# Kernel optimization log

Hardware: AMD Instinct MI355X
Metric: run time of the kernel (lower is better)

Reference implementation:

```python
import jax, jax.numpy as jnp
import numpy as np

SEQ = 4096
EMB = 2048
DQ = 2048
DV = 2048

def setup_inputs() -> dict:
    key = jax.random.key(0)
    k1, k2, k3, k4 = jax.random.split(key, 4)
    scale = 1.0 / np.sqrt(EMB)
    return {
        "embedding_word": jax.random.normal(k1, (SEQ, EMB), dtype=jnp.float32),
        "w_q": jax.random.normal(k2, (DQ, EMB), dtype=jnp.float32) * scale,
        "w_k": jax.random.normal(k3, (DQ, EMB), dtype=jnp.float32) * scale,
        "w_v": jax.random.normal(k4, (DV, EMB), dtype=jnp.float32) * scale,
    }

def reference(embedding_word, w_q, w_k, w_v):
    # nn.Linear: y = x @ W.T (bias=False)
    q = embedding_word @ w_q.T            # [S, d_q]
    k = embedding_word @ w_k.T            # [S, d_q]
    v = embedding_word @ w_v.T            # [S, d_v]
    scores = q @ k.T                      # [S, S]
    S = scores.shape[0]
    causal = jnp.tril(jnp.ones((S, S), dtype=bool))  # True = keep
    masked = jnp.where(causal, scores, -jnp.inf)
    weights = jax.nn.softmax(masked / jnp.sqrt(jnp.float32(DQ)), axis=-1)
    return weights @ v                    # [S, d_v]
```

## Files before the change

### kernel.cpp

```cpp
#include <hip/hip_runtime.h>


using u16 = unsigned short;
typedef __bf16 bf16x8 __attribute__((ext_vector_type(8)));
typedef float  f32x4  __attribute__((ext_vector_type(4)));
typedef u16    u16x8  __attribute__((ext_vector_type(8)));

__device__ __forceinline__ u16 f2b(float f) {
  union { float f; unsigned u; } x; x.f = f;
  unsigned r = x.u + 0x7fffu + ((x.u >> 16) & 1u);
  return (u16)(r >> 16);
}
__device__ __forceinline__ float b2f(u16 h) {
  union { unsigned u; float f; } x; x.u = ((unsigned)h) << 16;
  return x.f;
}

#define GLL16(src, dst)                                                        \
  __builtin_amdgcn_global_load_lds(                                            \
      (const __attribute__((address_space(1))) void*)(src),                    \
      (__attribute__((address_space(3))) void*)(dst), 16, 0, 0)

#define MFMA_BF16(a, b, c) __builtin_amdgcn_mfma_f32_16x16x32_bf16(a, b, c, 0, 0, 0)

__global__ __launch_bounds__(256)
void cast_all(const float* __restrict__ x, const float* __restrict__ wq,
              const float* __restrict__ wk, const float* __restrict__ wv,
              u16* __restrict__ dst) {
  const int b = blockIdx.x;
  const float* src;
  size_t off;
  if (b < 4096)      { src = x;  off = (size_t)b * 2048; }
  else if (b < 6144) { src = wq; off = (size_t)(b - 4096) * 2048; }
  else if (b < 8192) { src = wk; off = (size_t)(b - 6144) * 2048; }
  else               { src = wv; off = (size_t)(b - 8192) * 2048; }
  const size_t e = off + (size_t)threadIdx.x * 8;
  float4 a = *(const float4*)(src + e);
  float4 c = *(const float4*)(src + e + 4);
  u16x8 o;
  o[0] = f2b(a.x); o[1] = f2b(a.y); o[2] = f2b(a.z); o[3] = f2b(a.w);
  o[4] = f2b(c.x); o[5] = f2b(c.y); o[6] = f2b(c.z); o[7] = f2b(c.w);
  *(u16x8*)(dst + (size_t)b * 2048 + (size_t)threadIdx.x * 8) = o;
}

__global__ __launch_bounds__(512)
void gemm_qkv(const u16* __restrict__ A, const u16* __restrict__ W,
              u16* __restrict__ Qo, u16* __restrict__ Ko,
              u16* __restrict__ VTo, int bn_base) {
  extern __shared__ char lds[];
  constexpr int NT = 32;
  const int bn = blockIdx.x + bn_base, bm = blockIdx.y;
  const int tid = threadIdx.x;
  const int w = tid >> 6, lane = tid & 63;
  const int wr = w >> 1, wc = w & 1;
  const int l15 = lane & 15, l4 = lane >> 4;
  const int rs = lane >> 3;
  const int csw = ((lane & 7) ^ rs) << 3;
  const int m0 = bm * 256, n0 = bn * 128;

  const u16* gA = A + (size_t)(m0 + w * 8 + rs) * 2048 + csw;
  const u16* gB = W + (size_t)(n0 + w * 8 + rs) * 2048 + csw;
  char* lw = lds + w * 1024;
  const u16* sm = (const u16*)lds;

  auto stA = [&](int p, int u, int tt) {
    GLL16(gA + (size_t)u * 64 * 2048 + tt * 64, lw + p * 49152 + u * 8192);
  };
  auto stB = [&](int p, int u, int tt) {
    GLL16(gB + (size_t)u * 64 * 2048 + tt * 64, lw + p * 49152 + 32768 + u * 8192);
  };
  const int swz = (l15 & 7) << 3;
  auto rdA = [&](int p, int m, int kk) -> bf16x8 {
    int e = p * 24576 + wr * 4096 + (((m * 16 + l15) * 64 + kk * 32 + l4 * 8) ^ swz);
    return *(const bf16x8*)&sm[e];
  };
  auto rdB = [&](int p, int n, int kk) -> bf16x8 {
    int e = p * 24576 + 16384 + wc * 4096 +
            (((n * 16 + l15) * 64 + kk * 32 + l4 * 8) ^ swz);
    return *(const bf16x8*)&sm[e];
  };

  f32x4 acc[4][4] = {};
  bf16x8 aE[4][2], aO[4][2], b01E[2][2], b01O[2][2], b23E[2][2], b23O[2][2];

  stA(0,0,0); stA(0,1,0); stA(0,2,0); stA(0,3,0); stB(0,0,0); stB(0,1,0);
  stA(1,0,1); stA(1,1,1); stA(1,2,1); stA(1,3,1); stB(1,0,1); stB(1,1,1);
  asm volatile("s_waitcnt vmcnt(6)" ::: "memory");
  __builtin_amdgcn_sched_barrier(0);
  __builtin_amdgcn_s_barrier();
#pragma unroll
  for (int m = 0; m < 4; ++m) { aE[m][0] = rdA(0,m,0); aE[m][1] = rdA(0,m,1); }
#pragma unroll
  for (int n = 0; n < 2; ++n) { b01E[n][0] = rdB(0,n,0); b01E[n][1] = rdB(0,n,1); }
  asm volatile("s_waitcnt lgkmcnt(0)" ::: "memory");
  __builtin_amdgcn_sched_barrier(0);
  __builtin_amdgcn_s_barrier();

  for (int i = 0; i < NT / 2; ++i) {
    const int te = 2 * i, to = 2 * i + 1;
    if (te + 2 < NT) { stA(0,0,te+2); stA(0,1,te+2); stA(0,2,te+2); }
#pragma unroll
    for (int n = 0; n < 2; ++n) { b23E[n][0] = rdB(0,n+2,0); b23E[n][1] = rdB(0,n+2,1); }
    __builtin_amdgcn_s_barrier();
    __builtin_amdgcn_s_setprio(1);
#pragma unroll
    for (int m = 0; m < 4; ++m)
#pragma unroll
      for (int n = 0; n < 2; ++n)
#pragma unroll
        for (int kk = 0; kk < 2; ++kk)
          acc[m][n] = MFMA_BF16(aE[m][kk], b01E[n][kk], acc[m][n]);
    __builtin_amdgcn_s_setprio(0);
    asm volatile("s_waitcnt lgkmcnt(0)" ::: "memory");
    __builtin_amdgcn_sched_barrier(0);
    __builtin_amdgcn_s_barrier();
    if (te + 2 < NT) {
      stA(0,3,te+2); stB(0,0,te+2); stB(0,1,te+2);
      asm volatile("s_waitcnt vmcnt(6)" ::: "memory");
    } else {
      asm volatile("s_waitcnt vmcnt(0)" ::: "memory");
    }
    __builtin_amdgcn_sched_barrier(0);
    __builtin_amdgcn_s_barrier();
#pragma unroll
    for (int m = 0; m < 4; ++m) { aO[m][0] = rdA(1,m,0); aO[m][1] = rdA(1,m,1); }
#pragma unroll
    for (int n = 0; n < 2; ++n) { b01O[n][0] = rdB(1,n,0); b01O[n][1] = rdB(1,n,1); }
    __builtin_amdgcn_s_setprio(1);
#pragma unroll
    for (int m = 0; m < 4; ++m)
#pragma unroll
      for (int n = 0; n < 2; ++n)
#pragma unroll
        for (int kk = 0; kk < 2; ++kk)
          acc[m][n+2] = MFMA_BF16(aE[m][kk], b23E[n][kk], acc[m][n+2]);
    __builtin_amdgcn_s_setprio(0);
    asm volatile("s_waitcnt lgkmcnt(0)" ::: "memory");
    __builtin_amdgcn_sched_barrier(0);
    __builtin_amdgcn_s_barrier();
    if (to + 2 < NT) { stA(1,0,to+2); stA(1,1,to+2); stA(1,2,to+2); }
#pragma unroll
    for (int n = 0; n < 2; ++n) { b23O[n][0] = rdB(1,n+2,0); b23O[n][1] = rdB(1,n+2,1); }
    __builtin_amdgcn_s_barrier();
    __builtin_amdgcn_s_setprio(1);
#pragma unroll
    for (int m = 0; m < 4; ++m)
#pragma unroll
      for (int n = 0; n < 2; ++n)
#pragma unroll
        for (int kk = 0; kk < 2; ++kk)
          acc[m][n] = MFMA_BF16(aO[m][kk], b01O[n][kk], acc[m][n]);
    __builtin_amdgcn_s_setprio(0);
    asm volatile("s_waitcnt lgkmcnt(0)" ::: "memory");
    __builtin_amdgcn_sched_barrier(0);
    __builtin_amdgcn_s_barrier();
    if (to + 2 < NT) {
      stA(1,3,to+2); stB(1,0,to+2); stB(1,1,to+2);
      asm volatile("s_waitcnt vmcnt(6)" ::: "memory");
    } else if (to + 1 < NT) {
      asm volatile("s_waitcnt vmcnt(0)" ::: "memory");
    }
    __builtin_amdgcn_sched_barrier(0);
    __builtin_amdgcn_s_barrier();
    if (to + 1 < NT) {
#pragma unroll
      for (int m = 0; m < 4; ++m) { aE[m][0] = rdA(0,m,0); aE[m][1] = rdA(0,m,1); }
#pragma unroll
      for (int n = 0; n < 2; ++n) { b01E[n][0] = rdB(0,n,0); b01E[n][1] = rdB(0,n,1); }
    }
    __builtin_amdgcn_s_setprio(1);
#pragma unroll
    for (int m = 0; m < 4; ++m)
#pragma unroll
      for (int n = 0; n < 2; ++n)
#pragma unroll
        for (int kk = 0; kk < 2; ++kk)
          acc[m][n+2] = MFMA_BF16(aO[m][kk], b23O[n][kk], acc[m][n+2]);
    __builtin_amdgcn_s_setprio(0);
    asm volatile("s_waitcnt lgkmcnt(0)" ::: "memory");
    __builtin_amdgcn_sched_barrier(0);
    __builtin_amdgcn_s_barrier();
  }

  const int row0 = m0 + wr * 64 + l4 * 4;
  const int cg0 = n0 + wc * 64 + l15;
  if (bn < 16) {
#pragma unroll
    for (int m = 0; m < 4; ++m)
#pragma unroll
      for (int n = 0; n < 4; ++n)
#pragma unroll
        for (int j = 0; j < 4; ++j)
          Qo[(size_t)(row0 + m * 16 + j) * 2048 + cg0 + n * 16] = f2b(acc[m][n][j]);
  } else if (bn < 32) {
#pragma unroll
    for (int m = 0; m < 4; ++m)
#pragma unroll
      for (int n = 0; n < 4; ++n)
#pragma unroll
        for (int j = 0; j < 4; ++j)
          Ko[(size_t)(row0 + m * 16 + j) * 2048 + (cg0 + n * 16 - 2048)] = f2b(acc[m][n][j]);
  } else {
#pragma unroll
    for (int m = 0; m < 4; ++m)
#pragma unroll
      for (int n = 0; n < 4; ++n)
#pragma unroll
        for (int j = 0; j < 4; ++j)
          VTo[(size_t)(cg0 + n * 16 - 4096) * 4096 + row0 + m * 16 + j] = f2b(acc[m][n][j]);
  }
}

template<int MODE>
__global__ __launch_bounds__(256)
void pipe128(const u16* __restrict__ A, const u16* __restrict__ B,
             void* __restrict__ C, float alpha) {
  extern __shared__ char lds[];
  constexpr int LDA = (MODE == 0) ? 2048 : 4096;
  constexpr int LDB = (MODE == 0) ? 2048 : 4096;

  int bm, bn;
  if (MODE == 0) {
    const int b = blockIdx.x;
    int r = (int)((sqrtf(8.f * (float)b + 1.f) - 1.f) * 0.5f);
    while ((r + 1) * (r + 2) / 2 <= b) ++r;
    while (r * (r + 1) / 2 > b) --r;
    bm = r; bn = b - r * (r + 1) / 2;
  } else {
    const int b = blockIdx.x;
    bm = (b < 256) ? (b >> 4) : (31 - ((b - 256) >> 4));
    bn = b & 15;
  }
  const int NT = (MODE == 0) ? 32 : 2 * (bm + 1);

  const int tid = threadIdx.x;
  const int w = tid >> 6, lane = tid & 63;
  const int wr = w >> 1, wc = w & 1;
  const int l15 = lane & 15, l4 = lane >> 4;
  const int rs = lane >> 3;
  const int csw = ((lane & 7) ^ rs) << 3;
  const int m0 = bm * 128, n0 = bn * 128;

  const u16* gA = A + (size_t)(m0 + w * 8 + rs) * LDA + csw;
  const u16* gB = B + (size_t)(n0 + w * 8 + rs) * LDB + csw;
  char* lw = lds + w * 1024;
  const u16* sm = (const u16*)lds;

  auto stA = [&](int p, int u, int tt) {
    GLL16(gA + (size_t)(u * 32) * LDA + tt * 64, lw + p * 32768 + u * 4096);
  };
  auto stB = [&](int p, int u, int tt) {
    GLL16(gB + (size_t)(u * 32) * LDB + tt * 64, lw + p * 32768 + 16384 + u * 4096);
  };
  const int swz = (l15 & 7) << 3;
  auto rdA = [&](int p, int m, int kk) -> bf16x8 {
    int e = p * 16384 + wr * 4096 + (((m * 16 + l15) * 64 + kk * 32 + l4 * 8) ^ swz);
    return *(const bf16x8*)&sm[e];
  };
  auto rdB = [&](int p, int n, int kk) -> bf16x8 {
    int e = p * 16384 + 8192 + wc * 4096 +
            (((n * 16 + l15) * 64 + kk * 32 + l4 * 8) ^ swz);
    return *(const bf16x8*)&sm[e];
  };

  f32x4 acc[4][4] = {};
  bf16x8 aE[4][2], aO[4][2], b01E[2][2], b01O[2][2], b23E[2][2], b23O[2][2];

  stA(0,0,0); stA(0,1,0); stA(0,2,0); stA(0,3,0);
  stB(0,0,0); stB(0,1,0); stB(0,2,0); stB(0,3,0);
  stA(1,0,1); stA(1,1,1); stA(1,2,1); stA(1,3,1);
  stB(1,0,1); stB(1,1,1); stB(1,2,1); stB(1,3,1);
  asm volatile("s_waitcnt vmcnt(8)" ::: "memory");
  __builtin_amdgcn_sched_barrier(0);
  __builtin_amdgcn_s_barrier();
#pragma unroll
  for (int m = 0; m < 4; ++m) { aE[m][0] = rdA(0,m,0); aE[m][1] = rdA(0,m,1); }
#pragma unroll
  for (int n = 0; n < 2; ++n) { b01E[n][0] = rdB(0,n,0); b01E[n][1] = rdB(0,n,1); }
  asm volatile("s_waitcnt lgkmcnt(0)" ::: "memory");
  __builtin_amdgcn_sched_barrier(0);
  __builtin_amdgcn_s_barrier();

  for (int i = 0; i < (NT >> 1); ++i) {
    const int te = 2 * i, to = 2 * i + 1;
    if (te + 2 < NT) { stA(0,0,te+2); stA(0,1,te+2); stA(0,2,te+2); stA(0,3,te+2); }
#pragma unroll
    for (int n = 0; n < 2; ++n) { b23E[n][0] = rdB(0,n+2,0); b23E[n][1] = rdB(0,n+2,1); }
    __builtin_amdgcn_s_barrier();
    __builtin_amdgcn_s_setprio(1);
#pragma unroll
    for (int m = 0; m < 4; ++m)
#pragma unroll
      for (int n = 0; n < 2; ++n)
#pragma unroll
        for (int kk = 0; kk < 2; ++kk)
          acc[m][n] = MFMA_BF16(aE[m][kk], b01E[n][kk], acc[m][n]);
    __builtin_amdgcn_s_setprio(0);
    asm volatile("s_waitcnt lgkmcnt(0)" ::: "memory");
    __builtin_amdgcn_sched_barrier(0);
    __builtin_amdgcn_s_barrier();
    if (te + 2 < NT) {
      stB(0,0,te+2); stB(0,1,te+2); stB(0,2,te+2); stB(0,3,te+2);
      asm volatile("s_waitcnt vmcnt(8)" ::: "memory");
    } else {
      asm volatile("s_waitcnt vmcnt(0)" ::: "memory");
    }
    __builtin_amdgcn_sched_barrier(0);
    __builtin_amdgcn_s_barrier();
#pragma unroll
    for (int m = 0; m < 4; ++m) { aO[m][0] = rdA(1,m,0); aO[m][1] = rdA(1,m,1); }
#pragma unroll
    for (int n = 0; n < 2; ++n) { b01O[n][0] = rdB(1,n,0); b01O[n][1] = rdB(1,n,1); }
    __builtin_amdgcn_s_setprio(1);
#pragma unroll
    for (int m = 0; m < 4; ++m)
#pragma unroll
      for (int n = 0; n < 2; ++n)
#pragma unroll
        for (int kk = 0; kk < 2; ++kk)
          acc[m][n+2] = MFMA_BF16(aE[m][kk], b23E[n][kk], acc[m][n+2]);
    __builtin_amdgcn_s_setprio(0);
    asm volatile("s_waitcnt lgkmcnt(0)" ::: "memory");
    __builtin_amdgcn_sched_barrier(0);
    __builtin_amdgcn_s_barrier();
    if (to + 2 < NT) { stA(1,0,to+2); stA(1,1,to+2); stA(1,2,to+2); stA(1,3,to+2); }
#pragma unroll
    for (int n = 0; n < 2; ++n) { b23O[n][0] = rdB(1,n+2,0); b23O[n][1] = rdB(1,n+2,1); }
    __builtin_amdgcn_s_barrier();
    __builtin_amdgcn_s_setprio(1);
#pragma unroll
    for (int m = 0; m < 4; ++m)
#pragma unroll
      for (int n = 0; n < 2; ++n)
#pragma unroll
        for (int kk = 0; kk < 2; ++kk)
          acc[m][n] = MFMA_BF16(aO[m][kk], b01O[n][kk], acc[m][n]);
    __builtin_amdgcn_s_setprio(0);
    asm volatile("s_waitcnt lgkmcnt(0)" ::: "memory");
    __builtin_amdgcn_sched_barrier(0);
    __builtin_amdgcn_s_barrier();
    if (to + 2 < NT) {
      stB(1,0,to+2); stB(1,1,to+2); stB(1,2,to+2); stB(1,3,to+2);
      asm volatile("s_waitcnt vmcnt(8)" ::: "memory");
    } else if (to + 1 < NT) {
      asm volatile("s_waitcnt vmcnt(0)" ::: "memory");
    }
    __builtin_amdgcn_sched_barrier(0);
    __builtin_amdgcn_s_barrier();
    if (to + 1 < NT) {
#pragma unroll
      for (int m = 0; m < 4; ++m) { aE[m][0] = rdA(0,m,0); aE[m][1] = rdA(0,m,1); }
#pragma unroll
      for (int n = 0; n < 2; ++n) { b01E[n][0] = rdB(0,n,0); b01E[n][1] = rdB(0,n,1); }
    }
    __builtin_amdgcn_s_setprio(1);
#pragma unroll
    for (int m = 0; m < 4; ++m)
#pragma unroll
      for (int n = 0; n < 2; ++n)
#pragma unroll
        for (int kk = 0; kk < 2; ++kk)
          acc[m][n+2] = MFMA_BF16(aO[m][kk], b23O[n][kk], acc[m][n+2]);
    __builtin_amdgcn_s_setprio(0);
    asm volatile("s_waitcnt lgkmcnt(0)" ::: "memory");
    __builtin_amdgcn_sched_barrier(0);
    __builtin_amdgcn_s_barrier();
  }

  const int row0 = m0 + wr * 64 + l4 * 4;
  const int col0 = n0 + wc * 64 + l15;
  if (MODE == 0) {
    u16* Co = (u16*)C;
#pragma unroll
    for (int m = 0; m < 4; ++m)
#pragma unroll
      for (int n = 0; n < 4; ++n)
#pragma unroll
        for (int j = 0; j < 4; ++j)
          Co[(size_t)(row0 + m * 16 + j) * 4096 + col0 + n * 16] =
              f2b(acc[m][n][j] * alpha);
  } else {
    float* Co = (float*)C;
#pragma unroll
    for (int m = 0; m < 4; ++m)
#pragma unroll
      for (int n = 0; n < 4; ++n)
#pragma unroll
        for (int j = 0; j < 4; ++j)
          Co[(size_t)(row0 + m * 16 + j) * 2048 + col0 + n * 16] = acc[m][n][j];
  }
}

__global__ __launch_bounds__(256)
void softmax_causal(u16* __restrict__ S) {
  const int i = blockIdx.x;
  const int t = threadIdx.x;
  u16* row = S + (size_t)i * 4096;

  u16x8 r0 = *(const u16x8*)(row + t * 16);
  u16x8 r1 = *(const u16x8*)(row + t * 16 + 8);

  float v[16];
  float mx = -__builtin_inff();
#pragma unroll
  for (int c = 0; c < 16; ++c) {
    int j = t * 16 + c;
    float x = b2f(c < 8 ? r0[c] : r1[c - 8]);
    v[c] = (j <= i) ? x : -__builtin_inff();
    mx = fmaxf(mx, v[c]);
  }
#pragma unroll
  for (int off = 32; off >= 1; off >>= 1) mx = fmaxf(mx, __shfl_xor(mx, off));
  __shared__ float red[8];
  if ((t & 63) == 0) red[t >> 6] = mx;
  __syncthreads();
  mx = fmaxf(fmaxf(red[0], red[1]), fmaxf(red[2], red[3]));

  float s = 0.f;
#pragma unroll
  for (int c = 0; c < 16; ++c) {
    float e = exp2f((v[c] - mx) * 1.4426950408889634f);
    v[c] = e;
    s += e;
  }
#pragma unroll
  for (int off = 32; off >= 1; off >>= 1) s += __shfl_xor(s, off);
  if ((t & 63) == 0) red[4 + (t >> 6)] = s;
  __syncthreads();
  s = red[4] + red[5] + red[6] + red[7];
  float inv = 1.0f / s;

  u16x8 o0, o1;
#pragma unroll
  for (int c = 0; c < 8; ++c) {
    o0[c] = f2b(v[c] * inv);
    o1[c] = f2b(v[c + 8] * inv);
  }
  *(u16x8*)(row + t * 16) = o0;
  *(u16x8*)(row + t * 16 + 8) = o1;
}

extern "C" void kernel_launch(void* const* d_in, const int* in_sizes, int n_in,
                              void* d_out, int out_size, void* d_ws, size_t ws_size,
                              hipStream_t stream) {
  const float* x  = (const float*)d_in[0];
  const float* wq = (const float*)d_in[1];
  const float* wk = (const float*)d_in[2];
  const float* wv = (const float*)d_in[3];

  u16* x_bf  = (u16*)d_ws;
  u16* wq_bf = x_bf  + (size_t)4096 * 2048;
  u16* K_bf  = wq_bf + (size_t)3 * 2048 * 2048;
  u16* VT_bf = K_bf  + (size_t)4096 * 2048;
  u16* S_bf  = VT_bf + (size_t)2048 * 4096;
  u16* Q_bf  = (u16*)d_out;

  const float alpha = 0.022097086912079612f;

  cast_all<<<dim3(10240), 256, 0, stream>>>(x, wq, wk, wv, x_bf);

  gemm_qkv<<<dim3(32, 16), 512, 98304, stream>>>(x_bf, wq_bf, Q_bf, K_bf, VT_bf, 0);
  pipe128<0><<<dim3(528), 256, 65536, stream>>>(Q_bf, K_bf, S_bf, alpha);
  gemm_qkv<<<dim3(16, 16), 512, 98304, stream>>>(x_bf, wq_bf, Q_bf, K_bf, VT_bf, 32);
  softmax_causal<<<dim3(4096), 256, 0, stream>>>(S_bf);
  pipe128<1><<<dim3(512), 256, 65536, stream>>>(S_bf, VT_bf, d_out, 1.0f);
}
```

Measured before the change: 252.4 us.

## Use 256x256 tiles for Q/K projection and interleave PV block order

Adds a new Q/K projection GEMM kernel that computes 256x256 output tiles with 8 waves in a 2x4 layout, replacing the 256x128 tile launch. The larger tile raises arithmetic intensity and cuts the number of blocks from 512 to 256, at the cost of 128KB LDS per block and a larger accumulator register footprint. Separately, the weights@V kernel now alternates short and long causal row blocks in launch order to balance the load across CUs.

```diff
diff --git a/kernel.cpp b/kernel.cpp
--- a/kernel.cpp
+++ b/kernel.cpp
@@ -44,6 +44,146 @@
 }
 
 __global__ __launch_bounds__(512)
+void gemm_qk256(const u16* __restrict__ A, const u16* __restrict__ W,
+                u16* __restrict__ Qo, u16* __restrict__ Ko) {
+  extern __shared__ char lds[];
+  constexpr int NT = 32;
+  const int bn = blockIdx.x, bm = blockIdx.y;
+  const int tid = threadIdx.x;
+  const int w = tid >> 6, lane = tid & 63;
+  const int wr = w >> 2, wc = w & 3;
+  const int l15 = lane & 15, l4 = lane >> 4;
+  const int rs = lane >> 3;
+  const int csw = ((lane & 7) ^ rs) << 3;
+  const int m0 = bm * 256, n0 = bn * 256;
+
+  const u16* gA = A + (size_t)(m0 + w * 8 + rs) * 2048 + csw;
+  const u16* gB = W + (size_t)(n0 + w * 8 + rs) * 2048 + csw;
+  char* lw = lds + w * 1024;
+  const u16* sm = (const u16*)lds;
+
+  auto stA = [&](int p, int u, int tt) {
+    GLL16(gA + (size_t)(u * 64) * 2048 + tt * 64, lw + p * 65536 + u * 8192);
+  };
+  auto stB = [&](int p, int u, int tt) {
+    GLL16(gB + (size_t)(u * 64) * 2048 + tt * 64,
+          lw + p * 65536 + 32768 + u * 8192);
+  };
+  const int swz = (l15 & 7) << 3;
+  auto rdA = [&](int p, int m, int kk) -> bf16x8 {
+    int u = wr * 2 + (m >> 2);
+    int r64 = (m & 3) * 16 + l15;
+    int e = p * 32768 + u * 4096 + ((r64 * 64 + kk * 32 + l4 * 8) ^ swz);
+    return *(const bf16x8*)&sm[e];
+  };
+  auto rdB = [&](int p, int n, int kk) -> bf16x8 {
+    int e = p * 32768 + 16384 + wc * 4096 +
+            (((n * 16 + l15) * 64 + kk * 32 + l4 * 8) ^ swz);
+    return *(const bf16x8*)&sm[e];
+  };
+
+  f32x4 acc[8][4] = {};
+  bf16x8 a0[4][2], a1[4][2], b0[2][2], b1[2][2];
+
+  stA(0,0,0); stA(0,1,0); stA(0,2,0); stA(0,3,0);
+  stB(0,0,0); stB(0,1,0); stB(0,2,0); stB(0,3,0);
+  stA(1,0,1); stA(1,1,1); stA(1,2,1); stA(1,3,1);
+  stB(1,0,1); stB(1,1,1); stB(1,2,1); stB(1,3,1);
+  asm volatile("s_waitcnt vmcnt(8)" ::: "memory");
+  __builtin_amdgcn_sched_barrier(0);
+  __builtin_amdgcn_s_barrier();
+
+  for (int t = 0; t < NT; ++t) {
+    const int p = t & 1;
+    const bool pre = (t + 2 < NT);
+#pragma unroll
+    for (int m = 0; m < 4; ++m) { a0[m][0] = rdA(p, m, 0); a0[m][1] = rdA(p, m, 1); }
+#pragma unroll
+    for (int n = 0; n < 2; ++n) { b0[n][0] = rdB(p, n, 0); b0[n][1] = rdB(p, n, 1); }
+    __builtin_amdgcn_s_barrier();
+    asm volatile("s_waitcnt lgkmcnt(0)" ::: "memory");
+    __builtin_amdgcn_sched_barrier(0);
+    __builtin_amdgcn_s_setprio(1);
+#pragma unroll
+    for (int m = 0; m < 4; ++m)
+#pragma unroll
+      for (int n = 0; n < 2; ++n)
+#pragma unroll
+        for (int kk = 0; kk < 2; ++kk)
+          acc[m][n] = MFMA_BF16(a0[m][kk], b0[n][kk], acc[m][n]);
+    __builtin_amdgcn_s_setprio(0);
+    __builtin_amdgcn_s_barrier();
+    if (pre) { stA(p, 0, t + 2); stA(p, 2, t + 2); }
+#pragma unroll
+    for (int n = 0; n < 2; ++n) { b1[n][0] = rdB(p, n + 2, 0); b1[n][1] = rdB(p, n + 2, 1); }
+    __builtin_amdgcn_s_barrier();
+    asm volatile("s_waitcnt lgkmcnt(0)" ::: "memory");
+    __builtin_amdgcn_sched_barrier(0);
+    __builtin_amdgcn_s_setprio(1);
+#pragma unroll
+    for (int m = 0; m < 4; ++m)
+#pragma unroll
+      for (int n = 0; n < 2; ++n)
+#pragma unroll
+        for (int kk = 0; kk < 2; ++kk)
+          acc[m][n + 2] = MFMA_BF16(a0[m][kk], b1[n][kk], acc[m][n + 2]);
+    __builtin_amdgcn_s_setprio(0);
+    __builtin_amdgcn_s_barrier();
+    if (pre) { stB(p, 0, t + 2); stB(p, 1, t + 2); }
+#pragma unroll
+    for (int m = 0; m < 4; ++m) { a1[m][0] = rdA(p, m + 4, 0); a1[m][1] = rdA(p, m + 4, 1); }
+    __builtin_amdgcn_s_barrier();
+    asm volatile("s_waitcnt lgkmcnt(0)" ::: "memory");
+    __builtin_amdgcn_sched_barrier(0);
+    __builtin_amdgcn_s_setprio(1);
+#pragma unroll
+    for (int m = 0; m < 4; ++m)
+#pragma unroll
+      for (int n = 0; n < 2; ++n)
+#pragma unroll
+        for (int kk = 0; kk < 2; ++kk)
+          acc[m + 4][n] = MFMA_BF16(a1[m][kk], b0[n][kk], acc[m + 4][n]);
+    __builtin_amdgcn_s_setprio(0);
+    __builtin_amdgcn_s_barrier();
+    if (pre) { stA(p, 1, t + 2); stA(p, 3, t + 2); stB(p, 2, t + 2); stB(p, 3, t + 2); }
+    __builtin_amdgcn_s_setprio(1);
+#pragma unroll
+    for (int m = 0; m < 4; ++m)
+#pragma unroll
+      for (int n = 0; n < 2; ++n)
+#pragma unroll
+        for (int kk = 0; kk < 2; ++kk)
+          acc[m + 4][n + 2] = MFMA_BF16(a1[m][kk], b1[n][kk], acc[m + 4][n + 2]);
+    __builtin_amdgcn_s_setprio(0);
+    if (pre)                { asm volatile("s_waitcnt vmcnt(8)" ::: "memory"); }
+    else if (t + 1 < NT)    { asm volatile("s_waitcnt vmcnt(0)" ::: "memory"); }
+    __builtin_amdgcn_sched_barrier(0);
+    __builtin_amdgcn_s_barrier();
+  }
+
+  const int row0 = m0 + wr * 128 + l4 * 4;
+  if (bn < 8) {
+    const int cg0 = bn * 256 + wc * 64 + l15;
+#pragma unroll
+    for (int m = 0; m < 8; ++m)
+#pragma unroll
+      for (int n = 0; n < 4; ++n)
+#pragma unroll
+        for (int j = 0; j < 4; ++j)
+          Qo[(size_t)(row0 + m * 16 + j) * 2048 + cg0 + n * 16] = f2b(acc[m][n][j]);
+  } else {
+    const int cg0 = bn * 256 - 2048 + wc * 64 + l15;
+#pragma unroll
+    for (int m = 0; m < 8; ++m)
+#pragma unroll
+      for (int n = 0; n < 4; ++n)
+#pragma unroll
+        for (int j = 0; j < 4; ++j)
+          Ko[(size_t)(row0 + m * 16 + j) * 2048 + cg0 + n * 16] = f2b(acc[m][n][j]);
+  }
+}
+
+__global__ __launch_bounds__(512)
 void gemm_qkv(const u16* __restrict__ A, const u16* __restrict__ W,
               u16* __restrict__ Qo, u16* __restrict__ Ko,
               u16* __restrict__ VTo, int bn_base) {
@@ -228,8 +368,9 @@
     bm = r; bn = b - r * (r + 1) / 2;
   } else {
     const int b = blockIdx.x;
-    bm = (b < 256) ? (b >> 4) : (31 - ((b - 256) >> 4));
-    bn = b & 15;
+    const int i = b >> 1;
+    bm = (b & 1) ? (31 - (i >> 4)) : (i >> 4);
+    bn = i & 15;
   }
   const int NT = (MODE == 0) ? 32 : 2 * (bm + 1);
 
@@ -459,7 +600,7 @@
 
   cast_all<<<dim3(10240), 256, 0, stream>>>(x, wq, wk, wv, x_bf);
 
-  gemm_qkv<<<dim3(32, 16), 512, 98304, stream>>>(x_bf, wq_bf, Q_bf, K_bf, VT_bf, 0);
+  gemm_qk256<<<dim3(16, 16), 512, 131072, stream>>>(x_bf, wq_bf, Q_bf, K_bf);
   pipe128<0><<<dim3(528), 256, 65536, stream>>>(Q_bf, K_bf, S_bf, alpha);
   gemm_qkv<<<dim3(16, 16), 512, 98304, stream>>>(x_bf, wq_bf, Q_bf, K_bf, VT_bf, 32);
   softmax_causal<<<dim3(4096), 256, 0, stream>>>(S_bf);
```

Result: slower. 260.2 us (+3.1%).
